# Performance work log

Hardware: AMD Instinct MI355X
Metric: run time of the kernel (lower is better)

The kernel has to match this reference:

```python
import jax, jax.numpy as jnp
import numpy as np

B_SZ, SEQ, CH, ORDER = 8, 8192, 256, 64
EPS_LN = 1e-5
EPS_H = 1e-6


def setup_inputs() -> dict:
    key = jax.random.key(0)
    ks = jax.random.split(key, 12)
    s = 1.0 / np.sqrt(CH)
    x = jax.random.normal(ks[0], (B_SZ, SEQ, CH), jnp.float32)
    # RTF params: A = denominator coeffs (monic, leading 1 implied), B = numerator coeffs
    A = 0.01 * jax.random.normal(ks[1], (CH, ORDER), jnp.float32)  # small -> stable 1/A(z)
    Bp = 0.1 * jax.random.normal(ks[2], (CH, ORDER), jnp.float32)
    h0 = jnp.zeros((1,), jnp.float32)  # init torch.tensor([0.])
    W_enc = s * jax.random.normal(ks[3], (CH, CH), jnp.float32)
    b_enc = jnp.zeros((CH,), jnp.float32)
    W_fc = s * jax.random.normal(ks[4], (CH, CH), jnp.float32)
    b_fc = jnp.zeros((CH,), jnp.float32)
    gamma = jnp.ones((CH,), jnp.float32)
    beta = jnp.zeros((CH,), jnp.float32)
    W_dec = s * jax.random.normal(ks[5], (CH, CH), jnp.float32)
    b_dec = jnp.zeros((CH,), jnp.float32)
    return {"x": x, "A": A, "Bp": Bp, "h0": h0, "W_enc": W_enc, "b_enc": b_enc,
            "W_fc": W_fc, "b_fc": b_fc, "gamma": gamma, "beta": beta,
            "W_dec": W_dec, "b_dec": b_dec}


def _rtf_kernel(A, Bp, L):
    # K(z) = B(z)/A(z) with monic denominator a = [1, A_1..A_order]
    C = A.shape[0]
    a = jnp.concatenate([jnp.ones((C, 1), A.dtype), A], axis=1)  # (C, order+1)
    af = jnp.fft.rfft(a, n=L, axis=1)
    bf = jnp.fft.rfft(Bp, n=L, axis=1)
    return jnp.fft.irfft(bf / af, n=L, axis=1)  # (C, L)


def _causal_fft_conv(x, K):
    # x: (B, L, C); K: (C, L) per-channel causal filter
    L = x.shape[1]
    n = 2 * L
    xf = jnp.fft.rfft(x, n=n, axis=1)            # (B, n/2+1, C)
    Kf = jnp.fft.rfft(K.T, n=n, axis=0)          # (n/2+1, C)
    return jnp.fft.irfft(xf * Kf[None], n=n, axis=1)[:, :L]


def reference(x, A, Bp, h0, W_enc, b_enc, W_fc, b_fc, gamma, beta, W_dec, b_dec):
    gelu = lambda t: jax.nn.gelu(t, approximate=False)
    xe = x @ W_enc.T + b_enc                      # encode
    L = xe.shape[1]
    K = _rtf_kernel(A, Bp, L)                     # kernel generation from (A,B)
    h1 = _causal_fft_conv(xe, K)                  # FFT long convolution
    y1 = gelu(h1 + h0 * xe)                       # SSMRTF output (mult_activation=gelu)
    y2 = gelu(y1 @ W_fc.T + b_fc)                 # fc + final_act
    y2 = y2 + xe                                  # skip
    mu = jnp.mean(y2, axis=-1, keepdims=True)     # LayerNorm over channels
    var = jnp.mean(jnp.square(y2 - mu), axis=-1, keepdims=True)
    y2 = (y2 - mu) * jax.lax.rsqrt(var + EPS_LN) * gamma + beta
    y = y2 @ W_dec.T + b_dec                      # decode
    # h = ||y||_inf over seq / ||x_enc||_inf over seq
    h = jnp.max(jnp.abs(y), axis=1) / (jnp.max(jnp.abs(xe), axis=1) + EPS_H)
    return (y, h)
```

## Files before the change

### kernel.cpp

```cpp
#include <hip/hip_runtime.h>
#include <math.h>


#define BSZ   8
#define SEQ   8192
#define CHN   256
#define ORD   64
#define STAPS 512
#define NDD   17
#define PREPAD 544
#define XROW  (PREPAD + SEQ)
#define MTOT  (BSZ * SEQ)
#define YELEMS (MTOT * CHN)

#define CT2   1024
#define CTP   1032
#define CROW2 2048

typedef short s16x8 __attribute__((ext_vector_type(8)));
typedef float f32x4 __attribute__((ext_vector_type(4)));

#define MFMA16(a, b, c) __builtin_amdgcn_mfma_f32_16x16x32_bf16((a), (b), (c), 0, 0, 0)

__device__ __forceinline__ void gll16(const void* g, void* l) {
  __builtin_amdgcn_global_load_lds(
      (const __attribute__((address_space(1))) unsigned int*)g,
      (__attribute__((address_space(3))) unsigned int*)l, 16, 0, 0);
}

#define PERMC(row, h) (((row) * 8 + ((h) ^ ((row) & 7))) * 8)

__device__ __forceinline__ unsigned short f2bf(float f) {
  unsigned u = __float_as_uint(f);
  return (unsigned short)((u + 0x7FFFu + ((u >> 16) & 1u)) >> 16);
}
__device__ __forceinline__ float bf2f(unsigned short h) {
  return __uint_as_float(((unsigned)h) << 16);
}
__device__ __forceinline__ float geluf(float x) {
  float x2 = x * x;
  float y = x * __builtin_fmaf(0.0356774081f, x2, 0.7978845608f);
  float e = __builtin_amdgcn_exp2f(-2.8853900818f * y);
  return x * __builtin_amdgcn_rcpf(1.0f + e);
}
__device__ __forceinline__ uint4 packbf8(float4 a, float4 b) {
  uint4 r;
  r.x = (unsigned)f2bf(a.x) | ((unsigned)f2bf(a.y) << 16);
  r.y = (unsigned)f2bf(a.z) | ((unsigned)f2bf(a.w) << 16);
  r.z = (unsigned)f2bf(b.x) | ((unsigned)f2bf(b.y) << 16);
  r.w = (unsigned)f2bf(b.z) | ((unsigned)f2bf(b.w) << 16);
  return r;
}

__global__ __launch_bounds__(256) void k_pz(const float* we, const float* wf,
                                            const float* wd, unsigned short* owe,
                                            unsigned short* owf, unsigned short* owd,
                                            unsigned short* xeT, uint4* maxbufs) {
  int bx = blockIdx.x, tid = threadIdx.x;
  if (bx < 768) {
    int i = bx * 256 + tid;
    int which = i >> 16, off = i & 65535;
    if (which == 0)      owe[off] = f2bf(we[off]);
    else if (which == 1) owf[off] = f2bf(wf[off]);
    else                 owd[off] = f2bf(wd[off]);
  } else {
    int i = (bx - 768) * 256 + tid;
    uint4 z; z.x = 0; z.y = 0; z.z = 0; z.w = 0;
    if (i < 2048 * 68) {
      int row = i / 68, cc = i % 68;
      *(uint4*)((char*)xeT + (size_t)row * (XROW * 2) + (size_t)cc * 16) = z;
    } else {
      int j = i - 2048 * 68;
      if (j < 1024) maxbufs[j] = z;
    }
  }
}

__device__ __forceinline__ void kgen4(float* smemk, const float* A, const float* Bp,
                                      unsigned short* afr, int blk) {
  int tid = threadIdx.x, lane = tid & 63, wv = tid >> 6;
  int c = blk * 4 + wv;
  float* base = smemk + wv * 1872;
  float* G0 = base;
  float* G1 = base + 584;
  float* Et = base + 1168;
  float* Asl = base + 1232;
  float* Bsl = base + 1296;
  float* Kb = base + 1360;

  Asl[lane] = A[(size_t)c * ORD + lane];
  Bsl[lane] = Bp[(size_t)c * ORD + lane];
  for (int i = lane; i < 1168; i += 64) base[i] = 0.f;
  if (lane == 0) { G0[64] = 1.f; G1[65] = 1.f; }

  for (int n = 1; n < STAPS; n <<= 1) {
    int par = (n + lane) & 1;
    const float* Gc = par ? G1 : G0;
    int I0 = 64 + n + lane + par;
    float e0 = 0.f, e1 = 0.f, e2 = 0.f, e3 = 0.f;
#pragma unroll
    for (int g = 0; g < 16; ++g) {
      float4 av = *(const float4*)&Asl[4 * g];
      float2 vA = *(const float2*)&Gc[I0 - 4 * g - 2];
      float2 vB = *(const float2*)&Gc[I0 - 4 * g - 4];
      e0 += av.x * vA.y;
      e1 += av.y * vA.x;
      e2 += av.z * vB.y;
      e3 += av.w * vB.x;
    }
    Et[lane] = (e0 + e1) + (e2 + e3);
    int nk = (n + 63) >> 6;
    for (int k = 0; k < nk; ++k) {
      int idx = k * 64 + lane;
      int parU = (idx + 1) & 1;
      const float* Gu = parU ? G1 : G0;
      int J0 = 64 + idx - 1 + parU;
      float a0 = 0.f, a1 = 0.f, a2 = 0.f, a3 = 0.f;
#pragma unroll
      for (int g = 0; g < 16; ++g) {
        float4 ev = *(const float4*)&Et[4 * g];
        float2 vA = *(const float2*)&Gu[J0 - 4 * g];
        float2 vB = *(const float2*)&Gu[J0 - 4 * g - 2];
        a0 += ev.x * vA.y;
        a1 += ev.y * vA.x;
        a2 += ev.z * vB.y;
        a3 += ev.w * vB.x;
      }
      if (idx < n) {
        float gv = -((a0 + a1) + (a2 + a3));
        G0[64 + n + idx] = gv;
        G1[65 + n + idx] = gv;
      }
    }
  }

  for (int k = 0; k < 8; ++k) {
    int t = k * 64 + lane;
    int parB = (t + 1) & 1;
    const float* Gb = parB ? G1 : G0;
    int J0 = 64 + t - 1 + parB;
    float a0 = 0.f, a1 = 0.f, a2 = 0.f, a3 = 0.f;
#pragma unroll
    for (int g = 0; g < 16; ++g) {
      float4 bv = *(const float4*)&Bsl[4 * g];
      float2 vA = *(const float2*)&Gb[J0 - 4 * g];
      float2 vB = *(const float2*)&Gb[J0 - 4 * g - 2];
      a0 += bv.x * vA.y;
      a1 += bv.y * vA.x;
      a2 += bv.z * vB.y;
      a3 += bv.w * vB.x;
    }
    Kb[t] = (a0 + a1) + (a2 + a3);
  }

  int m = lane & 15, quad = lane >> 4;
  for (int dd = 0; dd < NDD; ++dd) {
    unsigned short v[8];
#pragma unroll
    for (int j = 0; j < 8; ++j) {
      int k = quad * 8 + j;
      int d = 2 * dd + (k >> 4);
      int p = k & 15;
      int s = 16 * d + m - p;
      float kv = (s >= 0 && s < STAPS) ? Kb[s] : 0.f;
      v[j] = f2bf(kv);
    }
    uint4 pk;
    pk.x = (unsigned)v[0] | ((unsigned)v[1] << 16);
    pk.y = (unsigned)v[2] | ((unsigned)v[3] << 16);
    pk.z = (unsigned)v[4] | ((unsigned)v[5] << 16);
    pk.w = (unsigned)v[6] | ((unsigned)v[7] << 16);
    *(uint4*)(afr + ((size_t)(c * NDD + dd) * 64 + lane) * 8) = pk;
  }
}

__global__ __launch_bounds__(256) void k_g1k(const float* A, const float* Bp,
                                             unsigned short* afr,
                                             const float* x, const unsigned short* wb,
                                             const float* benc, unsigned short* xeT,
                                             unsigned int* maxxe) {
  __shared__ __align__(16) char smem[40960];
  if (blockIdx.x < 64) {
    kgen4((float*)smem, A, Bp, afr, blockIdx.x);
    return;
  }
  unsigned short* As = (unsigned short*)smem;
  unsigned short* Bs = (unsigned short*)(smem + 32768);
  int tid = threadIdx.x, lane = tid & 63, wv = tid >> 6;
  int ln15 = lane & 15, hf = lane >> 4;
  size_t t0 = (size_t)(blockIdx.x - 64) * 64;
  int b = (int)(t0 >> 13), tin = (int)(t0 & 8191);
  f32x4 acc[4][4];
#pragma unroll
  for (int i = 0; i < 4; ++i)
#pragma unroll
    for (int j = 0; j < 4; ++j) { acc[i][j][0]=0.f; acc[i][j][1]=0.f; acc[i][j][2]=0.f; acc[i][j][3]=0.f; }

  for (int k0 = 0; k0 < CHN; k0 += 64) {
    __syncthreads();
#pragma unroll
    for (int i = 0; i < 8; ++i) {
      int p = 512 * wv + 64 * i + lane;
      int row = p >> 3, h = (p & 7) ^ (row & 7);
      gll16(wb + (size_t)row * CHN + k0 + h * 8, &As[(512 * wv + 64 * i) * 8]);
    }
    {
      int row = tid >> 2, hb = (tid & 3) * 2;
      const float* src = x + (t0 + row) * CHN + k0 + hb * 8;
      float4 f0 = *(const float4*)src;
      float4 f1 = *(const float4*)(src + 4);
      float4 f2 = *(const float4*)(src + 8);
      float4 f3 = *(const float4*)(src + 12);
      *(uint4*)&Bs[PERMC(row, hb)]     = packbf8(f0, f1);
      *(uint4*)&Bs[PERMC(row, hb + 1)] = packbf8(f2, f3);
    }
    __syncthreads();
#pragma unroll
    for (int ks = 0; ks < 2; ++ks) {
      s16x8 af[4], bfr[4];
#pragma unroll
      for (int mt = 0; mt < 4; ++mt) {
        int row = 64 * wv + 16 * mt + ln15;
        af[mt] = *(const s16x8*)&As[PERMC(row, ks * 4 + hf)];
      }
#pragma unroll
      for (int nt = 0; nt < 4; ++nt) {
        int row = 16 * nt + ln15;
        bfr[nt] = *(const s16x8*)&Bs[PERMC(row, ks * 4 + hf)];
      }
#pragma unroll
      for (int mt = 0; mt < 4; ++mt)
#pragma unroll
        for (int nt = 0; nt < 4; ++nt)
          acc[mt][nt] = MFMA16(af[mt], bfr[nt], acc[mt][nt]);
    }
  }
  int quad = hf;
#pragma unroll
  for (int mt = 0; mt < 4; ++mt) {
#pragma unroll
    for (int r = 0; r < 4; ++r) {
      int row = 64 * wv + 16 * mt + 4 * quad + r;
      float bias = benc[row];
      float mv = 0.f;
#pragma unroll
      for (int nt = 0; nt < 4; ++nt) {
        float v = acc[mt][nt][r] + bias;
        int t = tin + 16 * nt + ln15;
        xeT[(size_t)(b * CHN + row) * XROW + PREPAD + t] = f2bf(v);
        mv = fmaxf(mv, fabsf(v));
      }
      mv = fmaxf(mv, __shfl_xor(mv, 1)); mv = fmaxf(mv, __shfl_xor(mv, 2));
      mv = fmaxf(mv, __shfl_xor(mv, 4)); mv = fmaxf(mv, __shfl_xor(mv, 8));
      if (ln15 == 0) atomicMax(&maxxe[b * CHN + row], __float_as_uint(mv));
    }
  }
}

__global__ __launch_bounds__(512) void k_conv(const unsigned short* xeT,
                                              const unsigned short* afr,
                                              unsigned short* y1, const float* h0p) {
  __shared__ __align__(16) unsigned short xet[8 * CROW2];
  __shared__ __align__(16) unsigned short bnc[8 * CTP];
  int tid = threadIdx.x, lane = tid & 63, wv = tid >> 6;
  int idx = blockIdx.x;
  int tg = idx & 7, cg = (idx >> 3) & 31, b = idx >> 8;
  int c0 = cg * 8, t0 = tg * CT2;
  int c = c0 + wv;

  s16x8 afrg[NDD];
  {
    const unsigned short* ap = afr + (size_t)c * (NDD * 512) + (size_t)lane * 8;
#pragma unroll
    for (int dd = 0; dd < NDD; ++dd)
      afrg[dd] = *(const s16x8*)(ap + (size_t)dd * 512);
  }
  {
    int lp = lane ^ ((lane >> 3) & 7);
    const unsigned short* gbase = xeT + (size_t)(b * CHN + c) * XROW + t0;
    unsigned short* lbase = &xet[wv * CROW2];
#pragma unroll
    for (int k = 0; k < 4; ++k)
      gll16(gbase + (size_t)(64 * k + lp) * 8, &lbase[k * 64 * 8]);
  }
  float h0 = h0p[0];

  int n = lane & 15, quad = lane >> 4;
  int qc = quad - ((quad >> 1) << 2);
  const char* xb = (const char*)&xet[wv * CROW2];

  int ad[NDD];
  {
    int cb0 = 2 * n + qc + 68;
#pragma unroll
    for (int dd = 0; dd < NDD; ++dd) {
      int cc = cb0 - 4 * dd;
      ad[dd] = (cc ^ ((cc >> 3) & 7)) * 16;
    }
  }
  int ead;
  {
    int ch = 68 + 2 * n + (quad >> 1);
    ead = (ch ^ ((ch >> 3) & 7)) * 16 + 8 * (quad & 1);
  }
  __syncthreads();

#pragma unroll 1
  for (int s = 0; s < 4; ++s) {
    f32x4 a0, a1;
    a0[0]=0.f; a0[1]=0.f; a0[2]=0.f; a0[3]=0.f;
    a1[0]=0.f; a1[1]=0.f; a1[2]=0.f; a1[3]=0.f;
#pragma unroll
    for (int dd = 0; dd < 16; dd += 2) {
      a0 = MFMA16(afrg[dd],     *(const s16x8*)(xb + ad[dd]),     a0);
      a1 = MFMA16(afrg[dd + 1], *(const s16x8*)(xb + ad[dd + 1]), a1);
    }
    a0 = MFMA16(afrg[16], *(const s16x8*)(xb + ad[16]), a0);
    uint2 xvp = *(const uint2*)(xb + ead);
    unsigned short o[4];
#pragma unroll
    for (int r = 0; r < 4; ++r) {
      float xv = bf2f(((const unsigned short*)&xvp)[r]);
      float v = (a0[r] + a1[r]) + h0 * xv;
      o[r] = f2bf(geluf(v));
    }
    uint2 pw;
    pw.x = (unsigned)o[0] | ((unsigned)o[1] << 16);
    pw.y = (unsigned)o[2] | ((unsigned)o[3] << 16);
    *(uint2*)&bnc[wv * CTP + 256 * s + 16 * n + 4 * quad] = pw;
#pragma unroll
    for (int dd = 16; dd >= 8; --dd) ad[dd] = ad[dd - 8];
#pragma unroll
    for (int dd = 0; dd < 8; ++dd) ad[dd] = (ad[dd] + 512) ^ 64;
    ead = (ead + 512) ^ 64;
  }
  __syncthreads();
  {
    const size_t obase = (size_t)(b * SEQ + t0) * CHN + c0;
    int tb = tid >> 1, h = (tid & 1) * 4;
#pragma unroll
    for (int s = 0; s < 4; ++s) {
      int tl = 256 * s + tb;
      uint2 pk;
      pk.x = (unsigned)bnc[(h + 0) * CTP + tl] | ((unsigned)bnc[(h + 1) * CTP + tl] << 16);
      pk.y = (unsigned)bnc[(h + 2) * CTP + tl] | ((unsigned)bnc[(h + 3) * CTP + tl] << 16);
      *(uint2*)(y1 + obase + (size_t)tl * CHN + h) = pk;
    }
  }
}

__global__ __launch_bounds__(512) void k_gemm2(const unsigned short* y1,
                                               const unsigned short* wb, const float* bfc,
                                               const unsigned short* xeT, const float* gam,
                                               const float* bet, unsigned short* y2n) {
  __shared__ __align__(16) unsigned short Ws[256 * 64];
  __shared__ __align__(16) unsigned short Asb[128 * 64];
  __shared__ float pl[128][2][2];
  int tid = threadIdx.x, lane = tid & 63, wv = tid >> 6;
  int ln15 = lane & 15, hf = lane >> 4, quad = hf;
  size_t M0 = (size_t)blockIdx.x * 128;
  int b = (int)(M0 >> 13), tin = (int)(M0 & 8191);
  int mh = wv & 3, nh = wv >> 2;
  f32x4 acc[2][8];
#pragma unroll
  for (int i = 0; i < 2; ++i)
#pragma unroll
    for (int j = 0; j < 8; ++j) { acc[i][j][0]=0.f; acc[i][j][1]=0.f; acc[i][j][2]=0.f; acc[i][j][3]=0.f; }

  for (int k0 = 0; k0 < CHN; k0 += 64) {
    __syncthreads();
#pragma unroll
    for (int i = 0; i < 4; ++i) {
      int p = 256 * wv + 64 * i + lane;
      int row = p >> 3, h = (p & 7) ^ (row & 7);
      gll16(wb + (size_t)row * CHN + k0 + h * 8, &Ws[(256 * wv + 64 * i) * 8]);
    }
#pragma unroll
    for (int i = 0; i < 2; ++i) {
      int p = 128 * wv + 64 * i + lane;
      int row = p >> 3, h = (p & 7) ^ (row & 7);
      gll16(y1 + (M0 + row) * CHN + k0 + h * 8, &Asb[(128 * wv + 64 * i) * 8]);
    }
    __syncthreads();
#pragma unroll
    for (int ks = 0; ks < 2; ++ks) {
      s16x8 af[2], bfr[8];
#pragma unroll
      for (int mt = 0; mt < 2; ++mt) {
        int row = 32 * mh + 16 * mt + ln15;
        af[mt] = *(const s16x8*)&Asb[PERMC(row, ks * 4 + hf)];
      }
#pragma unroll
      for (int nt = 0; nt < 8; ++nt) {
        int row = 128 * nh + 16 * nt + ln15;
        bfr[nt] = *(const s16x8*)&Ws[PERMC(row, ks * 4 + hf)];
      }
#pragma unroll
      for (int mt = 0; mt < 2; ++mt)
#pragma unroll
        for (int nt = 0; nt < 8; ++nt)
          acc[mt][nt] = MFMA16(af[mt], bfr[nt], acc[mt][nt]);
    }
  }
  float g8[8], be8[8], bf8[8];
#pragma unroll
  for (int nt = 0; nt < 8; ++nt) {
    int col = 128 * nh + 16 * nt + ln15;
    g8[nt] = gam[col]; be8[nt] = bet[col]; bf8[nt] = bfc[col];
  }
#pragma unroll
  for (int mt = 0; mt < 2; ++mt) {
    int mlb = 32 * mh + 16 * mt + 4 * quad;
    uint2 xv2[8];
#pragma unroll
    for (int nt = 0; nt < 8; ++nt) {
      int col = 128 * nh + 16 * nt + ln15;
      xv2[nt] = *(const uint2*)(xeT + (size_t)(b * CHN + col) * XROW + PREPAD + tin + mlb);
    }
#pragma unroll
    for (int r = 0; r < 4; ++r) {
      int ml = mlb + r;
      float s1 = 0.f, s2 = 0.f;
#pragma unroll
      for (int nt = 0; nt < 8; ++nt) {
        float t2 = acc[mt][nt][r] + bf8[nt];
        float xv = bf2f(((const unsigned short*)&xv2[nt])[r]);
        float y2 = geluf(t2) + xv;
        acc[mt][nt][r] = y2;
        s1 += y2; s2 += y2 * y2;
      }
      s1 += __shfl_xor(s1, 1); s2 += __shfl_xor(s2, 1);
      s1 += __shfl_xor(s1, 2); s2 += __shfl_xor(s2, 2);
      s1 += __shfl_xor(s1, 4); s2 += __shfl_xor(s2, 4);
      s1 += __shfl_xor(s1, 8); s2 += __shfl_xor(s2, 8);
      if (ln15 == 0) { pl[ml][nh][0] = s1; pl[ml][nh][1] = s2; }
    }
  }
  __syncthreads();
#pragma unroll
  for (int mt = 0; mt < 2; ++mt) {
#pragma unroll
    for (int r = 0; r < 4; ++r) {
      int ml = 32 * mh + 16 * mt + 4 * quad + r;
      float s1 = pl[ml][0][0] + pl[ml][1][0];
      float s2 = pl[ml][0][1] + pl[ml][1][1];
      float mu = s1 * (1.f / 256.f);
      float var = s2 * (1.f / 256.f) - mu * mu;
      float ri = rsqrtf(var + 1e-5f);
#pragma unroll
      for (int nt = 0; nt < 8; ++nt) {
        int col = 128 * nh + 16 * nt + ln15;
        float yn = (acc[mt][nt][r] - mu) * ri * g8[nt] + be8[nt];
        y2n[(M0 + ml) * CHN + col] = f2bf(yn);
      }
    }
  }
}

__global__ __launch_bounds__(512) void k_gemm3(const unsigned short* y2n,
                                               const unsigned short* wb, const float* bd,
                                               float* yout, unsigned int* maxy) {
  __shared__ __align__(16) unsigned short Ws[256 * 64];
  __shared__ __align__(16) unsigned short Asb[128 * 64];
  int tid = threadIdx.x, lane = tid & 63, wv = tid >> 6;
  int ln15 = lane & 15, hf = lane >> 4, quad = hf;
  size_t M0 = (size_t)blockIdx.x * 128;
  int b = (int)(M0 >> 13);
  int mh = wv & 3, nh = wv >> 2;
  f32x4 acc[2][8];
#pragma unroll
  for (int i = 0; i < 2; ++i)
#pragma unroll
    for (int j = 0; j < 8; ++j) { acc[i][j][0]=0.f; acc[i][j][1]=0.f; acc[i][j][2]=0.f; acc[i][j][3]=0.f; }

  for (int k0 = 0; k0 < CHN; k0 += 64) {
    __syncthreads();
#pragma unroll
    for (int i = 0; i < 4; ++i) {
      int p = 256 * wv + 64 * i + lane;
      int row = p >> 3, h = (p & 7) ^ (row & 7);
      gll16(wb + (size_t)row * CHN + k0 + h * 8, &Ws[(256 * wv + 64 * i) * 8]);
    }
#pragma unroll
    for (int i = 0; i < 2; ++i) {
      int p = 128 * wv + 64 * i + lane;
      int row = p >> 3, h = (p & 7) ^ (row & 7);
      gll16(y2n + (M0 + row) * CHN + k0 + h * 8, &Asb[(128 * wv + 64 * i) * 8]);
    }
    __syncthreads();
#pragma unroll
    for (int ks = 0; ks < 2; ++ks) {
      s16x8 af[2], bfr[8];
#pragma unroll
      for (int mt = 0; mt < 2; ++mt) {
        int row = 32 * mh + 16 * mt + ln15;
        af[mt] = *(const s16x8*)&Asb[PERMC(row, ks * 4 + hf)];
      }
#pragma unroll
      for (int nt = 0; nt < 8; ++nt) {
        int row = 128 * nh + 16 * nt + ln15;
        bfr[nt] = *(const s16x8*)&Ws[PERMC(row, ks * 4 + hf)];
      }
#pragma unroll
      for (int mt = 0; mt < 2; ++mt)
#pragma unroll
        for (int nt = 0; nt < 8; ++nt)
          acc[mt][nt] = MFMA16(af[mt], bfr[nt], acc[mt][nt]);
    }
  }
  float bd8[8];
#pragma unroll
  for (int nt = 0; nt < 8; ++nt) bd8[nt] = bd[128 * nh + 16 * nt + ln15];
#pragma unroll
  for (int mt = 0; mt < 2; ++mt)
#pragma unroll
    for (int r = 0; r < 4; ++r) {
      int ml = 32 * mh + 16 * mt + 4 * quad + r;
#pragma unroll
      for (int nt = 0; nt < 8; ++nt) {
        int col = 128 * nh + 16 * nt + ln15;
        float v = acc[mt][nt][r] + bd8[nt];
        acc[mt][nt][r] = v;
        yout[(M0 + ml) * CHN + col] = v;
      }
    }
#pragma unroll
  for (int nt = 0; nt < 8; ++nt) {
    int col = 128 * nh + 16 * nt + ln15;
    float mv = 0.f;
#pragma unroll
    for (int mt = 0; mt < 2; ++mt)
#pragma unroll
      for (int r = 0; r < 4; ++r) mv = fmaxf(mv, fabsf(acc[mt][nt][r]));
    mv = fmaxf(mv, __shfl_xor(mv, 16));
    mv = fmaxf(mv, __shfl_xor(mv, 32));
    if (quad == 0) atomicMax(&maxy[b * CHN + col], __float_as_uint(mv));
  }
}

__global__ __launch_bounds__(256) void k_hfin(const unsigned int* maxxe,
                                              const unsigned int* maxy, float* hout) {
  int i = blockIdx.x * 256 + threadIdx.x;
  if (i < BSZ * CHN) {
    float mx = __uint_as_float(maxxe[i]);
    float my = __uint_as_float(maxy[i]);
    hout[i] = my / (mx + 1e-6f);
  }
}

extern "C" void kernel_launch(void* const* d_in, const int* in_sizes, int n_in,
                              void* d_out, int out_size, void* d_ws, size_t ws_size,
                              hipStream_t stream) {
  const float* x   = (const float*)d_in[0];
  const float* A   = (const float*)d_in[1];
  const float* Bp  = (const float*)d_in[2];
  const float* h0  = (const float*)d_in[3];
  const float* We  = (const float*)d_in[4];
  const float* be  = (const float*)d_in[5];
  const float* Wf  = (const float*)d_in[6];
  const float* bfc = (const float*)d_in[7];
  const float* gam = (const float*)d_in[8];
  const float* bet = (const float*)d_in[9];
  const float* Wd  = (const float*)d_in[10];
  const float* bd  = (const float*)d_in[11];

  char* ws = (char*)d_ws;
  unsigned short* y1  = (unsigned short*)(ws + 0);
  unsigned short* afr = (unsigned short*)(ws + 33554432);
  unsigned short* web = (unsigned short*)(ws + 38010880);
  unsigned short* wfb = (unsigned short*)(ws + 38141952);
  unsigned short* wdb = (unsigned short*)(ws + 38273024);
  unsigned int*  maxxe = (unsigned int*)(ws + 38404096);
  unsigned int*  maxy  = (unsigned int*)(ws + 38412288);

  unsigned short* xeT = (unsigned short*)d_out;
  float* yout = (float*)d_out;
  float* hout = yout + YELEMS;

  k_pz<<<1316, 256, 0, stream>>>(We, Wf, Wd, web, wfb, wdb, xeT, (uint4*)maxxe);
  k_g1k<<<1088, 256, 0, stream>>>(A, Bp, afr, x, web, be, xeT, maxxe);
  k_conv<<<2048, 512, 0, stream>>>(xeT, afr, y1, h0);
  k_gemm2<<<512, 512, 0, stream>>>(y1, wfb, bfc, xeT, gam, bet, y1);
  k_gemm3<<<512, 512, 0, stream>>>(y1, wdb, bd, yout, maxy);
  k_hfin<<<8, 256, 0, stream>>>(maxxe, maxy, hout);
}
```

Before: 282.7 us.

## Shrink prep kernel, fold weight casts and pad zeroing into encoder launch

The prep kernel now only casts W_enc (vectorised, 8 elements per thread) and clears the max buffers. Casting W_fc/W_dec and zeroing the xeT pre-pad rows move into extra blocks of the encoder/kernel-gen launch, so they run alongside the GEMM. Kernel generation now computes two channels per wave with only two waves active, which gives more independent work per thread but uses fewer waves per block. The aim is to cut the time of the serial prep launch and its scalar stores.

```diff
diff --git a/kernel.cpp b/kernel.cpp
--- a/kernel.cpp
+++ b/kernel.cpp
@@ -52,84 +52,86 @@
   return r;
 }
 
-__global__ __launch_bounds__(256) void k_pz(const float* we, const float* wf,
-                                            const float* wd, unsigned short* owe,
-                                            unsigned short* owf, unsigned short* owd,
-                                            unsigned short* xeT, uint4* maxbufs) {
+__global__ __launch_bounds__(256) void k_wenc(const float* we, unsigned short* web,
+                                              uint4* maxbufs) {
   int bx = blockIdx.x, tid = threadIdx.x;
-  if (bx < 768) {
-    int i = bx * 256 + tid;
-    int which = i >> 16, off = i & 65535;
-    if (which == 0)      owe[off] = f2bf(we[off]);
-    else if (which == 1) owf[off] = f2bf(wf[off]);
-    else                 owd[off] = f2bf(wd[off]);
+  if (bx < 32) {
+    int off = (bx * 256 + tid) * 8;
+    float4 f0 = *(const float4*)(we + off);
+    float4 f1 = *(const float4*)(we + off + 4);
+    *(uint4*)(web + off) = packbf8(f0, f1);
   } else {
-    int i = (bx - 768) * 256 + tid;
     uint4 z; z.x = 0; z.y = 0; z.z = 0; z.w = 0;
-    if (i < 2048 * 68) {
-      int row = i / 68, cc = i % 68;
-      *(uint4*)((char*)xeT + (size_t)row * (XROW * 2) + (size_t)cc * 16) = z;
-    } else {
-      int j = i - 2048 * 68;
-      if (j < 1024) maxbufs[j] = z;
-    }
-  }
-}
-
-__device__ __forceinline__ void kgen4(float* smemk, const float* A, const float* Bp,
-                                      unsigned short* afr, int blk) {
-  int tid = threadIdx.x, lane = tid & 63, wv = tid >> 6;
-  int c = blk * 4 + wv;
-  float* base = smemk + wv * 1872;
-  float* G0 = base;
-  float* G1 = base + 584;
-  float* Et = base + 1168;
-  float* Asl = base + 1232;
-  float* Bsl = base + 1296;
-  float* Kb = base + 1360;
-
-  Asl[lane] = A[(size_t)c * ORD + lane];
-  Bsl[lane] = Bp[(size_t)c * ORD + lane];
-  for (int i = lane; i < 1168; i += 64) base[i] = 0.f;
-  if (lane == 0) { G0[64] = 1.f; G1[65] = 1.f; }
+    maxbufs[(bx - 32) * 256 + tid] = z;
+  }
+}
+
+__device__ __forceinline__ void kgen2x(float* smemk, const float* A, const float* Bp,
+                                       unsigned short* afr, int blk) {
+  int tid = threadIdx.x;
+  if (tid >= 128) return;
+  int lane = tid & 63, wv = tid >> 6;
+  float* b0 = smemk + (size_t)(wv * 2) * 1872;
+  float* b1 = b0 + 1872;
+  int c0 = blk * 4 + wv * 2;
+
+  b0[1232 + lane] = A[(size_t)c0 * ORD + lane];
+  b1[1232 + lane] = A[(size_t)(c0 + 1) * ORD + lane];
+  b0[1296 + lane] = Bp[(size_t)c0 * ORD + lane];
+  b1[1296 + lane] = Bp[(size_t)(c0 + 1) * ORD + lane];
+  for (int i = lane; i < 1168; i += 64) { b0[i] = 0.f; b1[i] = 0.f; }
+  if (lane == 0) { b0[64] = 1.f; b0[584 + 65] = 1.f;
+                   b1[64] = 1.f; b1[584 + 65] = 1.f; }
 
   for (int n = 1; n < STAPS; n <<= 1) {
     int par = (n + lane) & 1;
-    const float* Gc = par ? G1 : G0;
+    int po = par ? 584 : 0;
     int I0 = 64 + n + lane + par;
-    float e0 = 0.f, e1 = 0.f, e2 = 0.f, e3 = 0.f;
+    const float* GA = b0 + po;
+    const float* GB = b1 + po;
+    float eA0=0.f,eA1=0.f,eA2=0.f,eA3=0.f, eB0=0.f,eB1=0.f,eB2=0.f,eB3=0.f;
 #pragma unroll
     for (int g = 0; g < 16; ++g) {
-      float4 av = *(const float4*)&Asl[4 * g];
-      float2 vA = *(const float2*)&Gc[I0 - 4 * g - 2];
-      float2 vB = *(const float2*)&Gc[I0 - 4 * g - 4];
-      e0 += av.x * vA.y;
-      e1 += av.y * vA.x;
-      e2 += av.z * vB.y;
-      e3 += av.w * vB.x;
-    }
-    Et[lane] = (e0 + e1) + (e2 + e3);
+      float4 avA = *(const float4*)&b0[1232 + 4 * g];
+      float4 avB = *(const float4*)&b1[1232 + 4 * g];
+      float2 vAA = *(const float2*)&GA[I0 - 4 * g - 2];
+      float2 vAB = *(const float2*)&GB[I0 - 4 * g - 2];
+      float2 vBA = *(const float2*)&GA[I0 - 4 * g - 4];
+      float2 vBB = *(const float2*)&GB[I0 - 4 * g - 4];
+      eA0 += avA.x * vAA.y;  eB0 += avB.x * vAB.y;
+      eA1 += avA.y * vAA.x;  eB1 += avB.y * vAB.x;
+      eA2 += avA.z * vBA.y;  eB2 += avB.z * vBB.y;
+      eA3 += avA.w * vBA.x;  eB3 += avB.w * vBB.x;
+    }
+    b0[1168 + lane] = (eA0 + eA1) + (eA2 + eA3);
+    b1[1168 + lane] = (eB0 + eB1) + (eB2 + eB3);
     int nk = (n + 63) >> 6;
     for (int k = 0; k < nk; ++k) {
       int idx = k * 64 + lane;
       int parU = (idx + 1) & 1;
-      const float* Gu = parU ? G1 : G0;
+      int pu = parU ? 584 : 0;
       int J0 = 64 + idx - 1 + parU;
-      float a0 = 0.f, a1 = 0.f, a2 = 0.f, a3 = 0.f;
+      const float* UA = b0 + pu;
+      const float* UB = b1 + pu;
+      float aA0=0.f,aA1=0.f,aA2=0.f,aA3=0.f, aB0=0.f,aB1=0.f,aB2=0.f,aB3=0.f;
 #pragma unroll
       for (int g = 0; g < 16; ++g) {
-        float4 ev = *(const float4*)&Et[4 * g];
-        float2 vA = *(const float2*)&Gu[J0 - 4 * g];
-        float2 vB = *(const float2*)&Gu[J0 - 4 * g - 2];
-        a0 += ev.x * vA.y;
-        a1 += ev.y * vA.x;
-        a2 += ev.z * vB.y;
-        a3 += ev.w * vB.x;
+        float4 evA = *(const float4*)&b0[1168 + 4 * g];
+        float4 evB = *(const float4*)&b1[1168 + 4 * g];
+        float2 vAA = *(const float2*)&UA[J0 - 4 * g];
+        float2 vAB = *(const float2*)&UB[J0 - 4 * g];
+        float2 vBA = *(const float2*)&UA[J0 - 4 * g - 2];
+        float2 vBB = *(const float2*)&UB[J0 - 4 * g - 2];
+        aA0 += evA.x * vAA.y;  aB0 += evB.x * vAB.y;
+        aA1 += evA.y * vAA.x;  aB1 += evB.y * vAB.x;
+        aA2 += evA.z * vBA.y;  aB2 += evB.z * vBB.y;
+        aA3 += evA.w * vBA.x;  aB3 += evB.w * vBB.x;
       }
       if (idx < n) {
-        float gv = -((a0 + a1) + (a2 + a3));
-        G0[64 + n + idx] = gv;
-        G1[65 + n + idx] = gv;
+        float gA = -((aA0 + aA1) + (aA2 + aA3));
+        float gB = -((aB0 + aB1) + (aB2 + aB3));
+        b0[64 + n + idx] = gA;  b0[584 + 65 + n + idx] = gA;
+        b1[64 + n + idx] = gB;  b1[584 + 65 + n + idx] = gB;
       }
     }
   }
@@ -137,40 +139,52 @@
   for (int k = 0; k < 8; ++k) {
     int t = k * 64 + lane;
     int parB = (t + 1) & 1;
-    const float* Gb = parB ? G1 : G0;
+    int pb = parB ? 584 : 0;
     int J0 = 64 + t - 1 + parB;
-    float a0 = 0.f, a1 = 0.f, a2 = 0.f, a3 = 0.f;
+    const float* PA = b0 + pb;
+    const float* PB = b1 + pb;
+    float aA0=0.f,aA1=0.f,aA2=0.f,aA3=0.f, aB0=0.f,aB1=0.f,aB2=0.f,aB3=0.f;
 #pragma unroll
     for (int g = 0; g < 16; ++g) {
-      float4 bv = *(const float4*)&Bsl[4 * g];
-      float2 vA = *(const float2*)&Gb[J0 - 4 * g];
-      float2 vB = *(const float2*)&Gb[J0 - 4 * g - 2];
-      a0 += bv.x * vA.y;
-      a1 += bv.y * vA.x;
-      a2 += bv.z * vB.y;
-      a3 += bv.w * vB.x;
-    }
-    Kb[t] = (a0 + a1) + (a2 + a3);
+      float4 bvA = *(const float4*)&b0[1296 + 4 * g];
+      float4 bvB = *(const float4*)&b1[1296 + 4 * g];
+      float2 vAA = *(const float2*)&PA[J0 - 4 * g];
+      float2 vAB = *(const float2*)&PB[J0 - 4 * g];
+      float2 vBA = *(const float2*)&PA[J0 - 4 * g - 2];
+      float2 vBB = *(const float2*)&PB[J0 - 4 * g - 2];
+      aA0 += bvA.x * vAA.y;  aB0 += bvB.x * vAB.y;
+      aA1 += bvA.y * vAA.x;  aB1 += bvB.y * vAB.x;
+      aA2 += bvA.z * vBA.y;  aB2 += bvB.z * vBB.y;
+      aA3 += bvA.w * vBA.x;  aB3 += bvB.w * vBB.x;
+    }
+    b0[1360 + t] = (aA0 + aA1) + (aA2 + aA3);
+    b1[1360 + t] = (aB0 + aB1) + (aB2 + aB3);
   }
 
   int m = lane & 15, quad = lane >> 4;
   for (int dd = 0; dd < NDD; ++dd) {
-    unsigned short v[8];
+    unsigned short vA[8], vB[8];
 #pragma unroll
     for (int j = 0; j < 8; ++j) {
       int k = quad * 8 + j;
       int d = 2 * dd + (k >> 4);
       int p = k & 15;
       int s = 16 * d + m - p;
-      float kv = (s >= 0 && s < STAPS) ? Kb[s] : 0.f;
-      v[j] = f2bf(kv);
-    }
-    uint4 pk;
-    pk.x = (unsigned)v[0] | ((unsigned)v[1] << 16);
-    pk.y = (unsigned)v[2] | ((unsigned)v[3] << 16);
-    pk.z = (unsigned)v[4] | ((unsigned)v[5] << 16);
-    pk.w = (unsigned)v[6] | ((unsigned)v[7] << 16);
-    *(uint4*)(afr + ((size_t)(c * NDD + dd) * 64 + lane) * 8) = pk;
+      bool ok = (s >= 0 && s < STAPS);
+      vA[j] = f2bf(ok ? b0[1360 + s] : 0.f);
+      vB[j] = f2bf(ok ? b1[1360 + s] : 0.f);
+    }
+    uint4 pkA, pkB;
+    pkA.x = (unsigned)vA[0] | ((unsigned)vA[1] << 16);
+    pkA.y = (unsigned)vA[2] | ((unsigned)vA[3] << 16);
+    pkA.z = (unsigned)vA[4] | ((unsigned)vA[5] << 16);
+    pkA.w = (unsigned)vA[6] | ((unsigned)vA[7] << 16);
+    pkB.x = (unsigned)vB[0] | ((unsigned)vB[1] << 16);
+    pkB.y = (unsigned)vB[2] | ((unsigned)vB[3] << 16);
+    pkB.z = (unsigned)vB[4] | ((unsigned)vB[5] << 16);
+    pkB.w = (unsigned)vB[6] | ((unsigned)vB[7] << 16);
+    *(uint4*)(afr + ((size_t)(c0 * NDD + dd) * 64 + lane) * 8) = pkA;
+    *(uint4*)(afr + ((size_t)((c0 + 1) * NDD + dd) * 64 + lane) * 8) = pkB;
   }
 }
 
@@ -178,17 +192,40 @@
                                              unsigned short* afr,
                                              const float* x, const unsigned short* wb,
                                              const float* benc, unsigned short* xeT,
-                                             unsigned int* maxxe) {
+                                             unsigned int* maxxe,
+                                             const float* wf, const float* wd,
+                                             unsigned short* wfb, unsigned short* wdb) {
   __shared__ __align__(16) char smem[40960];
   if (blockIdx.x < 64) {
-    kgen4((float*)smem, A, Bp, afr, blockIdx.x);
+    kgen2x((float*)smem, A, Bp, afr, blockIdx.x);
+    return;
+  }
+  if (blockIdx.x < 128) {
+    int gid = (blockIdx.x - 64) * 256 + threadIdx.x;
+    int mm = gid >> 13;
+    int off = (gid & 8191) * 8;
+    const float* src = (mm ? wd : wf) + off;
+    float4 f0 = *(const float4*)src;
+    float4 f1 = *(const float4*)(src + 4);
+    *(uint4*)((mm ? wdb : wfb) + off) = packbf8(f0, f1);
+    return;
+  }
+  if (blockIdx.x < 264) {
+    int j0 = (blockIdx.x - 128) * 1024 + threadIdx.x * 4;
+    uint4 z; z.x = 0; z.y = 0; z.z = 0; z.w = 0;
+#pragma unroll
+    for (int u = 0; u < 4; ++u) {
+      int j = j0 + u;
+      int row = j / 68, cc = j % 68;
+      *(uint4*)((char*)xeT + (size_t)row * (XROW * 2) + (size_t)cc * 16) = z;
+    }
     return;
   }
   unsigned short* As = (unsigned short*)smem;
   unsigned short* Bs = (unsigned short*)(smem + 32768);
   int tid = threadIdx.x, lane = tid & 63, wv = tid >> 6;
   int ln15 = lane & 15, hf = lane >> 4;
-  size_t t0 = (size_t)(blockIdx.x - 64) * 64;
+  size_t t0 = (size_t)(blockIdx.x - 264) * 64;
   int b = (int)(t0 >> 13), tin = (int)(t0 & 8191);
   f32x4 acc[4][4];
 #pragma unroll
@@ -577,8 +614,9 @@
   float* yout = (float*)d_out;
   float* hout = yout + YELEMS;
 
-  k_pz<<<1316, 256, 0, stream>>>(We, Wf, Wd, web, wfb, wdb, xeT, (uint4*)maxxe);
-  k_g1k<<<1088, 256, 0, stream>>>(A, Bp, afr, x, web, be, xeT, maxxe);
+  k_wenc<<<36, 256, 0, stream>>>(We, web, (uint4*)maxxe);
+  k_g1k<<<1288, 256, 0, stream>>>(A, Bp, afr, x, web, be, xeT, maxxe,
+                                  Wf, Wd, wfb, wdb);
   k_conv<<<2048, 512, 0, stream>>>(xeT, afr, y1, h0);
   k_gemm2<<<512, 512, 0, stream>>>(y1, wfb, bfc, xeT, gam, bet, y1);
   k_gemm3<<<512, 512, 0, stream>>>(y1, wdb, bd, yout, maxy);
```

New measurement: 311.6 us. 1.1x slower.
